# Kernel optimization log

Hardware: AMD Instinct MI355X
Metric: run time of the kernel (lower is better)

## Reference

```python
import jax, jax.numpy as jnp
import numpy as np

N = 100000      # num_nodes
D = 128         # emb_size
LYR = 3         # num_layers
E = 1600000     # num edges (avg degree 16)
Q = 100000      # num label pairs to score


def setup_inputs() -> dict:
    key = jax.random.key(0)
    ks = jax.random.split(key, 8)
    xavier = float(np.sqrt(6.0 / (D + D)))  # xavier_uniform bound for square Linear
    return {
        "edge_index": jax.random.randint(ks[0], (2, E), 0, N),
        "edge_label_index": jax.random.randint(ks[1], (2, Q), 0, N),
        "edge_weight": jax.random.uniform(ks[2], (E,), dtype=jnp.float32),
        "emb": jax.random.uniform(ks[3], (N, D), dtype=jnp.float32, minval=-xavier, maxval=xavier),
        "gc_w": jax.random.uniform(ks[4], (LYR, D, D), dtype=jnp.float32, minval=-xavier, maxval=xavier),
        "gc_b": jnp.zeros((LYR, D), dtype=jnp.float32),
        "bi_w": jax.random.uniform(ks[5], (LYR, D, D), dtype=jnp.float32, minval=-xavier, maxval=xavier),
        "bi_b": jnp.zeros((LYR, D), dtype=jnp.float32),
        "num_nodes": N,
    }


def _get_embedding(edge_index, edge_weight, emb, gc_w, gc_b, bi_w, bi_b, num_nodes):
    row, col = edge_index[0], edge_index[1]
    ego = emb                      # [N, D]
    all_embs = [ego]
    for i in range(gc_w.shape[0]):
        # sparse adj @ ego: out[row] += w * ego[col]
        msg = jax.ops.segment_sum(edge_weight[:, None] * ego[col], row,
                                  num_segments=num_nodes)          # [N, D]
        aggr = msg @ gc_w[i].T + gc_b[i]                            # Linear (torch: x @ W.T + b)
        bi = (ego * msg) @ bi_w[i].T + bi_b[i]
        ego = jax.nn.leaky_relu(aggr + bi, negative_slope=0.2)      # eval mode: dropout = identity
        norm = ego / jnp.maximum(
            jnp.linalg.norm(ego, axis=1, keepdims=True), 1e-12)    # F.normalize(p=2, dim=1)
        all_embs.append(norm)
    return jnp.concatenate(all_embs, axis=1)                        # [N, (L+1)*D]


def reference(edge_index, edge_label_index, edge_weight, emb, gc_w, gc_b, bi_w, bi_b, num_nodes):
    all_embs = _get_embedding(edge_index, edge_weight, emb, gc_w, gc_b, bi_w, bi_b, num_nodes)
    out_src = all_embs[edge_label_index[0]]   # [Q, (L+1)*D]
    out_dst = all_embs[edge_label_index[1]]
    return jnp.sum(out_src * out_dst, axis=-1)  # [Q]
```

## Files before the change

### kernel.cpp

```cpp
#include <hip/hip_runtime.h>

#define DD 128
#define K2 256
#define NBMAX 1024
#define COLMASK 0x01FFFFFF
#define SCAP 4096

typedef short short8 __attribute__((ext_vector_type(8)));
typedef float f32x4  __attribute__((ext_vector_type(4)));
typedef unsigned int uint4v __attribute__((ext_vector_type(4)));

static inline size_t align256(size_t x){ return (x + 255) & ~(size_t)255; }

__device__ __forceinline__ unsigned short f2bf(float x){
  unsigned int u = __builtin_bit_cast(unsigned int, x);
  u += 0x7fff + ((u >> 16) & 1);
  return (unsigned short)(u >> 16);
}
__device__ __forceinline__ float bf2f(unsigned short h){
  unsigned int u = ((unsigned int)h) << 16;
  return __builtin_bit_cast(float, u);
}

__device__ __forceinline__ short8 prod8(short8 mv, short8 ev){
  short8 r;
#pragma unroll
  for (int u = 0; u < 8; u++){
    float p = bf2f((unsigned short)mv[u]) * bf2f((unsigned short)ev[u]);
    r[u] = (short)f2bf(p);
  }
  return r;
}

__device__ __forceinline__ int2 ntload_i2(const int2* p){
  unsigned long long v = __builtin_nontemporal_load((const unsigned long long*)p);
  return make_int2((int)(unsigned int)v, (int)(unsigned int)(v >> 32));
}

__device__ __forceinline__ void acc8(float* a, uint4v v, float w){
#pragma unroll
  for (int j = 0; j < 4; j++){
    unsigned int u = v[j];
    a[2*j]   = fmaf(w, bf2f((unsigned short)u), a[2*j]);
    a[2*j+1] = fmaf(w, bf2f((unsigned short)(u >> 16)), a[2*j+1]);
  }
}

__global__ __launch_bounds__(256) void bucket_hist_kernel(
    const int* __restrict__ ei, int E, int* __restrict__ bcnt, int NB){
  __shared__ int lh[NBMAX];
  int t = threadIdx.x;
  int base = blockIdx.x * 8192;
  for (int j = t; j < NB; j += 256) lh[j] = 0;
  __syncthreads();
#pragma unroll
  for (int i = 0; i < 32; i++){
    int e = base + i*256 + t;
    if (e < E) atomicAdd(&lh[ei[e] >> 7], 1);
  }
  __syncthreads();
  for (int j = t; j < NB; j += 256){
    int c = lh[j];
    if (c) atomicAdd(&bcnt[j], c);
  }
}

__global__ __launch_bounds__(1024) void bucket_scan_kernel(
    const int* __restrict__ bcnt, int* __restrict__ bbase, int* __restrict__ bcur, int NB){
  __shared__ int a[NBMAX], btmp[NBMAX];
  int t = threadIdx.x;
  a[t] = (t < NB) ? bcnt[t] : 0;
  __syncthreads();
  int* src = a; int* dst = btmp;
  for (int o = 1; o < 1024; o <<= 1){
    int val = src[t];
    if (t >= o) val += src[t - o];
    dst[t] = val;
    __syncthreads();
    int* tm = src; src = dst; dst = tm;
  }
  int excl = (t == 0) ? 0 : src[t-1];
  if (t < NB){ bbase[t] = excl; bcur[t] = excl; }
}

__global__ __launch_bounds__(256) void fill_binned_kernel(
    const int* __restrict__ ei, const float* __restrict__ ew, int E,
    int* __restrict__ bcur, int2* __restrict__ csre, int NB){
  __shared__ int lhist[NBMAX];
  __shared__ int lbase[NBMAX];
  int t = threadIdx.x;
  int base = blockIdx.x * 4096;
  for (int j = t; j < NB; j += 256) lhist[j] = 0;
  __syncthreads();
  int rows[16];
#pragma unroll
  for (int i = 0; i < 16; i++){
    int e = base + i*256 + t;
    int r = (e < E) ? ei[e] : -1;
    rows[i] = r;
    if (r >= 0) atomicAdd(&lhist[r >> 7], 1);
  }
  __syncthreads();
  for (int j = t; j < NB; j += 256){
    int c = lhist[j];
    lbase[j] = c ? atomicAdd(&bcur[j], c) : 0;
    lhist[j] = 0;
  }
  __syncthreads();
#pragma unroll
  for (int i = 0; i < 16; i++){
    int e = base + i*256 + t;
    int r = rows[i];
    if (r >= 0){
      int b = r >> 7;
      int pos = lbase[b] + atomicAdd(&lhist[b], 1);
      int col = ei[E + e];
      float w = ew[e];
      csre[pos] = make_int2(((r & 127) << 25) | col, __float_as_int(w));
    }
  }
}

__global__ __launch_bounds__(256) void bucket_rowdeg_kernel(
    const int* __restrict__ bbase, const int* __restrict__ bcur,
    const int2* __restrict__ csre, int* __restrict__ deg, int* __restrict__ psum, int N){
  __shared__ int lc[128];
  __shared__ int red[128];
  int b = blockIdx.x, t = threadIdx.x;
  if (t < 128) lc[t] = 0;
  __syncthreads();
  int beg = bbase[b], end = bcur[b];
  for (int i = beg + t; i < end; i += 256)
    atomicAdd(&lc[((unsigned int)csre[i].x) >> 25], 1);
  __syncthreads();
  int gr = b*128 + t;
  int d = 0;
  if (t < 128 && gr < N){ d = lc[t]; deg[gr] = d; }
  if (t < 128) red[t] = (d + 7) & ~7;
  __syncthreads();
  for (int o = 64; o > 0; o >>= 1){
    if (t < o) red[t] += red[t+o];
    __syncthreads();
  }
  if (t == 0) psum[b] = red[0];
}

__global__ __launch_bounds__(1024) void pscan_kernel(
    const int* __restrict__ psum, int* __restrict__ pbase, int* __restrict__ rowptrN, int NB){
  __shared__ int a[NBMAX], btmp[NBMAX];
  int t = threadIdx.x;
  a[t] = (t < NB) ? psum[t] : 0;
  __syncthreads();
  int* src = a; int* dst = btmp;
  for (int o = 1; o < 1024; o <<= 1){
    int val = src[t];
    if (t >= o) val += src[t - o];
    dst[t] = val;
    __syncthreads();
    int* tm = src; src = dst; dst = tm;
  }
  int excl = (t == 0) ? 0 : src[t-1];
  if (t < NB) pbase[t] = excl;
  if (t == NB-1) *rowptrN = excl + psum[t];
}

__global__ __launch_bounds__(256) void sortbkt_kernel(
    const int* __restrict__ pbase, const int* __restrict__ bbase, const int* __restrict__ bcur,
    const int* __restrict__ deg, const int2* __restrict__ csre, int2* __restrict__ csre2,
    int* __restrict__ rowptr, int N){
  __shared__ int2 obuf[SCAP];
  __shared__ int lrp[129];
  __shared__ int lcur[128];
  __shared__ int sa[128], sb[128];
  int b = blockIdx.x;
  int t = threadIdx.x;
  int r0 = b*128;
  int gr = r0 + t;
  int d = (t < 128 && gr < N) ? deg[gr] : 0;
  if (t < 128){ sa[t] = (d + 7) & ~7; lcur[t] = 0; }
  __syncthreads();
  int* s0 = sa; int* s1 = sb;
  for (int o = 1; o < 128; o <<= 1){
    if (t < 128){
      int v = s0[t];
      if (t >= o) v += s0[t - o];
      s1[t] = v;
    }
    __syncthreads();
    int* tm = s0; s0 = s1; s1 = tm;
  }
  int pb = pbase[b];
  if (t < 128){
    int excl = t ? s0[t-1] : 0;
    lrp[t] = pb + excl;
    if (gr < N) rowptr[gr] = pb + excl;
    if (t == 127) lrp[128] = pb + s0[127];
  }
  __syncthreads();

  int gb = lrp[0];
  int outLen = lrp[128] - gb;
  int beg = bbase[b], bend = bcur[b];
  const int2 pad = make_int2(0, 0);

  if (outLen <= SCAP){
    for (int i = beg + t; i < bend; i += 256){
      int2 e = csre[i];
      int rl = ((unsigned int)e.x) >> 25;
      int pos = lrp[rl] - gb + atomicAdd(&lcur[rl], 1);
      obuf[pos] = e;
    }
    if (t < 128 && gr < N){
      int pbg = lrp[t] - gb + d, pe = lrp[t+1] - gb;
      for (int i = pbg; i < pe; i++) obuf[i] = pad;
    }
    __syncthreads();
    for (int i = t; i < outLen; i += 256) csre2[gb + i] = obuf[i];
  } else {
    for (int i = beg + t; i < bend; i += 256){
      int2 e = csre[i];
      int rl = ((unsigned int)e.x) >> 25;
      int pos = lrp[rl] + atomicAdd(&lcur[rl], 1);
      csre2[pos] = e;
    }
    __syncthreads();
    if (t < 128 && gr < N){
      int pbeg = lrp[t] + lcur[t];
      int pend = lrp[t+1];
      for (int i = pbeg; i < pend; i++) csre2[i] = pad;
    }
  }
}

__global__ void pack_cvt_kernel(const float* __restrict__ gcw, const float* __restrict__ biw,
                                unsigned short* __restrict__ wb, int LYR,
                                const float* __restrict__ emb, unsigned int* __restrict__ feat4u,
                                int n2, int fsU){
  int i = blockIdx.x*blockDim.x + threadIdx.x;
  int wtotal = LYR*DD*K2;
  if (i < wtotal){
    int l = i / (DD*K2);
    int r = i - l*(DD*K2);
    int n = r >> 8;
    int k = r & (K2-1);
    float v = (k < DD) ? gcw[(size_t)l*DD*DD + n*DD + k]
                       : biw[(size_t)l*DD*DD + n*DD + (k - DD)];
    wb[i] = f2bf(v);
    return;
  }
  int j = i - wtotal;
  if (j < n2){
    float2 v = *(const float2*)(emb + (size_t)j*2);
    int n = j >> 6, c = j & 63;
    feat4u[(size_t)n*fsU + c] = (unsigned int)f2bf(v.x) | ((unsigned int)f2bf(v.y) << 16);
  }
}

__global__ void gather_kernel(const int* __restrict__ rowptr, const int2* __restrict__ csre,
                              const unsigned short* __restrict__ feat, int fs,
                              unsigned int* __restrict__ msgh, int N){
  int wid = (int)(((size_t)blockIdx.x*blockDim.x + threadIdx.x) >> 6);
  int lane = threadIdx.x & 63;
  if (wid >= N) return;
  int g  = lane >> 4;
  int fl = lane & 15;
  int beg = rowptr[wid], end = rowptr[wid+1];
  const unsigned short* fbase = feat + fl*8;
  float a[8];
#pragma unroll
  for (int i = 0; i < 8; i++) a[i] = 0.f;

  const int2* ep = csre + beg + g;
  int k = beg;
  for (; k + 16 <= end; k += 16){
    int2 e0 = ntload_i2(ep);
    int2 e1 = ntload_i2(ep + 4);
    int2 e2 = ntload_i2(ep + 8);
    int2 e3 = ntload_i2(ep + 12);
    uint4v v0 = *(const uint4v*)(fbase + (size_t)(e0.x & COLMASK)*fs);
    uint4v v1 = *(const uint4v*)(fbase + (size_t)(e1.x & COLMASK)*fs);
    uint4v v2 = *(const uint4v*)(fbase + (size_t)(e2.x & COLMASK)*fs);
    uint4v v3 = *(const uint4v*)(fbase + (size_t)(e3.x & COLMASK)*fs);
    acc8(a, v0, __int_as_float(e0.y));
    acc8(a, v1, __int_as_float(e1.y));
    acc8(a, v2, __int_as_float(e2.y));
    acc8(a, v3, __int_as_float(e3.y));
    ep += 16;
  }
  for (; k < end; k += 8){
    int2 e0 = ntload_i2(ep);
    int2 e1 = ntload_i2(ep + 4);
    uint4v v0 = *(const uint4v*)(fbase + (size_t)(e0.x & COLMASK)*fs);
    uint4v v1 = *(const uint4v*)(fbase + (size_t)(e1.x & COLMASK)*fs);
    acc8(a, v0, __int_as_float(e0.y));
    acc8(a, v1, __int_as_float(e1.y));
    ep += 8;
  }

#pragma unroll
  for (int i = 0; i < 8; i++){
    a[i] += __shfl_xor(a[i], 16, 64);
    a[i] += __shfl_xor(a[i], 32, 64);
  }
  if (g == 0){
    uint4v o;
    o.x = (unsigned int)f2bf(a[0]) | ((unsigned int)f2bf(a[1]) << 16);
    o.y = (unsigned int)f2bf(a[2]) | ((unsigned int)f2bf(a[3]) << 16);
    o.z = (unsigned int)f2bf(a[4]) | ((unsigned int)f2bf(a[5]) << 16);
    o.w = (unsigned int)f2bf(a[6]) | ((unsigned int)f2bf(a[7]) << 16);
    *(uint4v*)(msgh + (size_t)wid*(DD/2) + fl*4) = o;
  }
}

__global__ __launch_bounds__(256) void transform_mfma_kernel(
    const unsigned short* __restrict__ ego_in, const unsigned short* __restrict__ msgh,
    int fs, const unsigned short* __restrict__ wb, const float* __restrict__ gcb,
    const float* __restrict__ bib, unsigned short* __restrict__ ego_out,
    float* __restrict__ nscale, int N){
  int t = threadIdx.x;
  int wave = t >> 6, lane = t & 63;
  int m = lane & 15, q = lane >> 4;
  int wr0 = blockIdx.x * 64 + wave * 16;

  float bias[8];
#pragma unroll
  for (int ct = 0; ct < 8; ct++) bias[ct] = gcb[ct*16 + m] + bib[ct*16 + m];

  int row0 = wr0 + m;
  int cr0 = row0 < N ? row0 : N-1;
  const unsigned short* mrow0 = msgh   + (size_t)cr0*DD;
  const unsigned short* erow0 = ego_in + (size_t)cr0*fs;
  const unsigned short* wrow  = wb + (size_t)m*K2;

  short8 mv[4], ev[4];
#pragma unroll
  for (int cc = 0; cc < 4; cc++){
    int c = cc*32 + q*8;
    mv[cc] = *(const short8*)(mrow0 + c);
    ev[cc] = *(const short8*)(erow0 + c);
  }
  short8 pv[4];
#pragma unroll
  for (int cc = 0; cc < 4; cc++) pv[cc] = prod8(mv[cc], ev[cc]);

  f32x4 acc[8];
#pragma unroll
  for (int ct = 0; ct < 8; ct++) acc[ct] = (f32x4)0.f;

#pragma unroll
  for (int cc = 0; cc < 4; cc++){
    int c = cc*32 + q*8;
#pragma unroll
    for (int ct = 0; ct < 8; ct++){
      short8 bm = *(const short8*)(wrow + (size_t)ct*16*K2 + c);
      short8 bp = *(const short8*)(wrow + (size_t)ct*16*K2 + DD + c);
      acc[ct] = __builtin_amdgcn_mfma_f32_16x16x32_bf16(mv[cc], bm, acc[ct], 0, 0, 0);
      acc[ct] = __builtin_amdgcn_mfma_f32_16x16x32_bf16(pv[cc], bp, acc[ct], 0, 0, 0);
    }
  }

#pragma unroll
  for (int reg = 0; reg < 4; reg++){
    int gr = wr0 + q*4 + reg;
    float rs = 0.f;
#pragma unroll
    for (int ct = 0; ct < 8; ct++){
      float x = acc[ct][reg] + bias[ct];
      x = (x > 0.f) ? x : 0.2f*x;
      rs += x*x;
      if (gr < N) ego_out[(size_t)gr*fs + ct*16 + m] = f2bf(x);
    }
#pragma unroll
    for (int o = 1; o < 16; o <<= 1) rs += __shfl_xor(rs, o, 16);
    if (m == 0 && gr < N)
      nscale[(size_t)gr*3] = 1.0f / fmaxf(sqrtf(rs), 1e-12f);
  }
}

__global__ void score_all_kernel(const int* __restrict__ eli, int Q,
                                 const unsigned int* __restrict__ feat4u, int fsU,
                                 const float* __restrict__ nsall,
                                 float* __restrict__ out){
  int wid = (int)(((size_t)blockIdx.x*blockDim.x + threadIdx.x) >> 6);
  int lane = threadIdx.x & 63;
  if (wid >= Q) return;
  int s = eli[wid];
  int d = eli[Q + wid];
  int g = lane >> 4;
  uint4v a = *(const uint4v*)(feat4u + (size_t)s*fsU + lane*4);
  uint4v b = *(const uint4v*)(feat4u + (size_t)d*fsU + lane*4);
  int so = g ? (g - 1) : 0;
  float ls = nsall[(size_t)s*3 + so];
  float ld = nsall[(size_t)d*3 + so];
  float p = 0.f;
#pragma unroll
  for (int j = 0; j < 4; j++){
    p += bf2f((unsigned short)a[j]) * bf2f((unsigned short)b[j]);
    p += bf2f((unsigned short)(a[j] >> 16)) * bf2f((unsigned short)(b[j] >> 16));
  }
  if (g) p *= ls * ld;
  for (int o = 32; o > 0; o >>= 1) p += __shfl_xor(p, o, 64);
  if (lane == 0) out[wid] = p;
}

extern "C" void kernel_launch(void* const* d_in, const int* in_sizes, int n_in,
                              void* d_out, int out_size, void* d_ws, size_t ws_size,
                              hipStream_t stream){
  const int*   edge_index = (const int*)d_in[0];
  const int*   eli        = (const int*)d_in[1];
  const float* ew         = (const float*)d_in[2];
  const float* emb        = (const float*)d_in[3];
  const float* gcw        = (const float*)d_in[4];
  const float* gcb        = (const float*)d_in[5];
  const float* biw        = (const float*)d_in[6];
  const float* bib        = (const float*)d_in[7];
  const int E   = in_sizes[2];
  const int Q   = in_sizes[1] / 2;
  const int N   = in_sizes[3] / DD;
  const int LYR = in_sizes[4] / (DD*DD);
  float* out = (float*)d_out;

  const int FS  = (LYR + 1) * DD;
  const int FSU = FS / 2;

  char* base = (char*)d_ws;
  size_t off = 0;
  auto carve = [&](size_t bytes)->char*{
    char* r = base + off;
    off = align256(off + bytes);
    return r;
  };

  unsigned short* feat4  = (unsigned short*) carve((size_t)N*FS*sizeof(unsigned short));
  size_t msgB_ = (size_t)N*DD*sizeof(unsigned short);
  size_t csreB_ = (size_t)E*sizeof(int2);
  unsigned short* msgh   = (unsigned short*) carve(msgB_ > csreB_ ? msgB_ : csreB_);
  int2*           csre   = (int2*)msgh;
  unsigned short* wb     = (unsigned short*) carve((size_t)LYR*DD*K2*sizeof(unsigned short));
  float*          nsall  = (float*)          carve((size_t)3*N*sizeof(float));
  int*            rowptr = (int*)            carve((size_t)(N+1)*sizeof(int));
  int*            deg    = (int*)            carve((size_t)N*sizeof(int));
  int*            bcnt   = (int*)            carve((size_t)NBMAX*sizeof(int));
  int*            bbase  = (int*)            carve((size_t)NBMAX*sizeof(int));
  int*            bcur   = (int*)            carve((size_t)NBMAX*sizeof(int));
  int*            psum   = (int*)            carve((size_t)NBMAX*sizeof(int));
  int*            pbase  = (int*)            carve((size_t)NBMAX*sizeof(int));
  int2*           csre2  = (int2*)           carve(((size_t)E + 7*(size_t)N + 8)*sizeof(int2));
  (void)n_in; (void)out_size; (void)ws_size;

  const int NB = (N + 127)/128;

  hipMemsetAsync(bcnt, 0, (size_t)NB*sizeof(int), stream);
  bucket_hist_kernel<<<(E + 8191)/8192, 256, 0, stream>>>(edge_index, E, bcnt, NB);
  bucket_scan_kernel<<<1, 1024, 0, stream>>>(bcnt, bbase, bcur, NB);
  fill_binned_kernel<<<(E + 4095)/4096, 256, 0, stream>>>(edge_index, ew, E, bcur, csre, NB);
  bucket_rowdeg_kernel<<<NB, 256, 0, stream>>>(bbase, bcur, csre, deg, psum, N);
  pscan_kernel<<<1, 1024, 0, stream>>>(psum, pbase, rowptr + N, NB);
  sortbkt_kernel<<<NB, 256, 0, stream>>>(pbase, bbase, bcur, deg, csre, csre2, rowptr, N);
  {
    int total = LYR*DD*K2 + N*DD/2;
    pack_cvt_kernel<<<(total + 255)/256, 256, 0, stream>>>(
        gcw, biw, wb, LYR, emb, (unsigned int*)feat4, N*DD/2, FSU);
  }

  for (int l = 0; l < LYR; l++){
    int blocks = (int)(((size_t)N*64 + 255)/256);
    gather_kernel<<<blocks, 256, 0, stream>>>(rowptr, csre2, feat4 + (size_t)l*DD, FS,
                                              (unsigned int*)msgh, N);
    transform_mfma_kernel<<<(N + 63)/64, 256, 0, stream>>>(
        feat4 + (size_t)l*DD, msgh, FS, wb + (size_t)l*DD*K2,
        gcb + (size_t)l*DD, bib + (size_t)l*DD,
        feat4 + (size_t)(l+1)*DD, nsall + l, N);
  }
  {
    int blocks = (int)(((size_t)Q*64 + 255)/256);
    score_all_kernel<<<blocks, 256, 0, stream>>>(eli, Q, (const unsigned int*)feat4, FSU,
                                                 nsall, out);
  }
}
```

Baseline: 586.0 us.

## Fuse neighbor gather with MFMA transform per layer via LDS message tile

Merges the per-layer gather and transform kernels into one kernel. Each wave gathers 16 rows sequentially and writes the bf16 messages into an XOR-swizzled LDS tile, which the MFMA transform then reads directly. This removes the global msgh round trip and one launch per layer. The cost is fewer waves in flight during the gather (one wave per 16 rows instead of one per row), which can reduce memory-level parallelism for the latency-bound gather.

```diff
diff --git a/kernel.cpp b/kernel.cpp
--- a/kernel.cpp
+++ b/kernel.cpp
@@ -256,93 +256,90 @@
   }
 }
 
-__global__ void gather_kernel(const int* __restrict__ rowptr, const int2* __restrict__ csre,
-                              const unsigned short* __restrict__ feat, int fs,
-                              unsigned int* __restrict__ msgh, int N){
-  int wid = (int)(((size_t)blockIdx.x*blockDim.x + threadIdx.x) >> 6);
-  int lane = threadIdx.x & 63;
-  if (wid >= N) return;
-  int g  = lane >> 4;
-  int fl = lane & 15;
-  int beg = rowptr[wid], end = rowptr[wid+1];
-  const unsigned short* fbase = feat + fl*8;
-  float a[8];
-#pragma unroll
-  for (int i = 0; i < 8; i++) a[i] = 0.f;
-
-  const int2* ep = csre + beg + g;
-  int k = beg;
-  for (; k + 16 <= end; k += 16){
-    int2 e0 = ntload_i2(ep);
-    int2 e1 = ntload_i2(ep + 4);
-    int2 e2 = ntload_i2(ep + 8);
-    int2 e3 = ntload_i2(ep + 12);
-    uint4v v0 = *(const uint4v*)(fbase + (size_t)(e0.x & COLMASK)*fs);
-    uint4v v1 = *(const uint4v*)(fbase + (size_t)(e1.x & COLMASK)*fs);
-    uint4v v2 = *(const uint4v*)(fbase + (size_t)(e2.x & COLMASK)*fs);
-    uint4v v3 = *(const uint4v*)(fbase + (size_t)(e3.x & COLMASK)*fs);
-    acc8(a, v0, __int_as_float(e0.y));
-    acc8(a, v1, __int_as_float(e1.y));
-    acc8(a, v2, __int_as_float(e2.y));
-    acc8(a, v3, __int_as_float(e3.y));
-    ep += 16;
-  }
-  for (; k < end; k += 8){
-    int2 e0 = ntload_i2(ep);
-    int2 e1 = ntload_i2(ep + 4);
-    uint4v v0 = *(const uint4v*)(fbase + (size_t)(e0.x & COLMASK)*fs);
-    uint4v v1 = *(const uint4v*)(fbase + (size_t)(e1.x & COLMASK)*fs);
-    acc8(a, v0, __int_as_float(e0.y));
-    acc8(a, v1, __int_as_float(e1.y));
-    ep += 8;
-  }
-
-#pragma unroll
-  for (int i = 0; i < 8; i++){
-    a[i] += __shfl_xor(a[i], 16, 64);
-    a[i] += __shfl_xor(a[i], 32, 64);
-  }
-  if (g == 0){
-    uint4v o;
-    o.x = (unsigned int)f2bf(a[0]) | ((unsigned int)f2bf(a[1]) << 16);
-    o.y = (unsigned int)f2bf(a[2]) | ((unsigned int)f2bf(a[3]) << 16);
-    o.z = (unsigned int)f2bf(a[4]) | ((unsigned int)f2bf(a[5]) << 16);
-    o.w = (unsigned int)f2bf(a[6]) | ((unsigned int)f2bf(a[7]) << 16);
-    *(uint4v*)(msgh + (size_t)wid*(DD/2) + fl*4) = o;
-  }
-}
-
-__global__ __launch_bounds__(256) void transform_mfma_kernel(
-    const unsigned short* __restrict__ ego_in, const unsigned short* __restrict__ msgh,
-    int fs, const unsigned short* __restrict__ wb, const float* __restrict__ gcb,
+__global__ __launch_bounds__(256) void layer_fused_kernel(
+    const int* __restrict__ rowptr, const int2* __restrict__ csre,
+    const unsigned short* __restrict__ feat, int fs,
+    const unsigned short* __restrict__ wb, const float* __restrict__ gcb,
     const float* __restrict__ bib, unsigned short* __restrict__ ego_out,
     float* __restrict__ nscale, int N){
+  __shared__ unsigned short lmsg[4*2048];
   int t = threadIdx.x;
   int wave = t >> 6, lane = t & 63;
+  int g = lane >> 4, fl = lane & 15;
+  int wr0 = blockIdx.x * 64 + wave * 16;
+  unsigned short* ms = lmsg + wave*2048;
+
+  int ridx = wr0 + fl; if (ridx > N-1) ridx = N-1;
+  int rp0 = rowptr[ridx], rp1 = rowptr[ridx+1];
+
+  const unsigned short* fbase = feat + fl*8;
+  for (int r = 0; r < 16; r++){
+    int beg = __shfl(rp0, r, 64);
+    int end = __shfl(rp1, r, 64);
+    float a[8];
+#pragma unroll
+    for (int i = 0; i < 8; i++) a[i] = 0.f;
+    const int2* ep = csre + beg + g;
+    int k = beg;
+    for (; k + 16 <= end; k += 16){
+      int2 e0 = ntload_i2(ep);
+      int2 e1 = ntload_i2(ep + 4);
+      int2 e2 = ntload_i2(ep + 8);
+      int2 e3 = ntload_i2(ep + 12);
+      uint4v v0 = *(const uint4v*)(fbase + (size_t)(e0.x & COLMASK)*fs);
+      uint4v v1 = *(const uint4v*)(fbase + (size_t)(e1.x & COLMASK)*fs);
+      uint4v v2 = *(const uint4v*)(fbase + (size_t)(e2.x & COLMASK)*fs);
+      uint4v v3 = *(const uint4v*)(fbase + (size_t)(e3.x & COLMASK)*fs);
+      acc8(a, v0, __int_as_float(e0.y));
+      acc8(a, v1, __int_as_float(e1.y));
+      acc8(a, v2, __int_as_float(e2.y));
+      acc8(a, v3, __int_as_float(e3.y));
+      ep += 16;
+    }
+    for (; k < end; k += 8){
+      int2 e0 = ntload_i2(ep);
+      int2 e1 = ntload_i2(ep + 4);
+      uint4v v0 = *(const uint4v*)(fbase + (size_t)(e0.x & COLMASK)*fs);
+      uint4v v1 = *(const uint4v*)(fbase + (size_t)(e1.x & COLMASK)*fs);
+      acc8(a, v0, __int_as_float(e0.y));
+      acc8(a, v1, __int_as_float(e1.y));
+      ep += 8;
+    }
+#pragma unroll
+    for (int i = 0; i < 8; i++){
+      a[i] += __shfl_xor(a[i], 16, 64);
+      a[i] += __shfl_xor(a[i], 32, 64);
+    }
+    if (g == 0){
+      uint4v o;
+      o.x = (unsigned int)f2bf(a[0]) | ((unsigned int)f2bf(a[1]) << 16);
+      o.y = (unsigned int)f2bf(a[2]) | ((unsigned int)f2bf(a[3]) << 16);
+      o.z = (unsigned int)f2bf(a[4]) | ((unsigned int)f2bf(a[5]) << 16);
+      o.w = (unsigned int)f2bf(a[6]) | ((unsigned int)f2bf(a[7]) << 16);
+      *(uint4v*)&ms[r*128 + ((fl*8) ^ ((r&7)<<3))] = o;
+    }
+  }
+
   int m = lane & 15, q = lane >> 4;
-  int wr0 = blockIdx.x * 64 + wave * 16;
-
-  float bias[8];
-#pragma unroll
-  for (int ct = 0; ct < 8; ct++) bias[ct] = gcb[ct*16 + m] + bib[ct*16 + m];
+  short8 mv[4];
+#pragma unroll
+  for (int cc = 0; cc < 4; cc++)
+    mv[cc] = *(const short8*)&ms[m*128 + ((cc*32 + q*8) ^ ((m&7)<<3))];
 
   int row0 = wr0 + m;
   int cr0 = row0 < N ? row0 : N-1;
-  const unsigned short* mrow0 = msgh   + (size_t)cr0*DD;
-  const unsigned short* erow0 = ego_in + (size_t)cr0*fs;
-  const unsigned short* wrow  = wb + (size_t)m*K2;
-
-  short8 mv[4], ev[4];
-#pragma unroll
-  for (int cc = 0; cc < 4; cc++){
-    int c = cc*32 + q*8;
-    mv[cc] = *(const short8*)(mrow0 + c);
-    ev[cc] = *(const short8*)(erow0 + c);
-  }
-  short8 pv[4];
+  const unsigned short* erow0 = feat + (size_t)cr0*fs;
+  short8 ev[4], pv[4];
+#pragma unroll
+  for (int cc = 0; cc < 4; cc++) ev[cc] = *(const short8*)(erow0 + cc*32 + q*8);
 #pragma unroll
   for (int cc = 0; cc < 4; cc++) pv[cc] = prod8(mv[cc], ev[cc]);
 
+  float bias[8];
+#pragma unroll
+  for (int ct = 0; ct < 8; ct++) bias[ct] = gcb[ct*16 + m] + bib[ct*16 + m];
+
+  const unsigned short* wrow = wb + (size_t)m*K2;
   f32x4 acc[8];
 #pragma unroll
   for (int ct = 0; ct < 8; ct++) acc[ct] = (f32x4)0.f;
@@ -432,10 +429,8 @@
   };
 
   unsigned short* feat4  = (unsigned short*) carve((size_t)N*FS*sizeof(unsigned short));
-  size_t msgB_ = (size_t)N*DD*sizeof(unsigned short);
   size_t csreB_ = (size_t)E*sizeof(int2);
-  unsigned short* msgh   = (unsigned short*) carve(msgB_ > csreB_ ? msgB_ : csreB_);
-  int2*           csre   = (int2*)msgh;
+  int2*           csre   = (int2*)           carve(csreB_);
   unsigned short* wb     = (unsigned short*) carve((size_t)LYR*DD*K2*sizeof(unsigned short));
   float*          nsall  = (float*)          carve((size_t)3*N*sizeof(float));
   int*            rowptr = (int*)            carve((size_t)(N+1)*sizeof(int));
@@ -464,12 +459,9 @@
   }
 
   for (int l = 0; l < LYR; l++){
-    int blocks = (int)(((size_t)N*64 + 255)/256);
-    gather_kernel<<<blocks, 256, 0, stream>>>(rowptr, csre2, feat4 + (size_t)l*DD, FS,
-                                              (unsigned int*)msgh, N);
-    transform_mfma_kernel<<<(N + 63)/64, 256, 0, stream>>>(
-        feat4 + (size_t)l*DD, msgh, FS, wb + (size_t)l*DD*K2,
-        gcb + (size_t)l*DD, bib + (size_t)l*DD,
+    layer_fused_kernel<<<(N + 63)/64, 256, 0, stream>>>(
+        rowptr, csre2, feat4 + (size_t)l*DD, FS,
+        wb + (size_t)l*DD*K2, gcb + (size_t)l*DD, bib + (size_t)l*DD,
         feat4 + (size_t)(l+1)*DD, nsall + l, N);
   }
   {
```

After: 632.0 us. 7.8% more time.
